# Kernel optimization log

Measured on AMD Instinct MI355X. Metric: run time of the kernel, lower is better.

The kernel has to match this reference:

```python
import jax, jax.numpy as jnp
import numpy as np

QMAX = 255.0  # bit=8 unsigned activation range


def ste_round(x):
    # straight-through round: exact integer rounding in fwd, identity grad
    return x + jax.lax.stop_gradient(jnp.round(x) - x)


def conv3x3(x, w, stride=1):
    return jax.lax.conv_general_dilated(
        x, w, window_strides=(stride, stride), padding=((1, 1), (1, 1)),
        dimension_numbers=('NCHW', 'OIHW', 'NCHW'))


def setup_inputs() -> dict:
    key = jax.random.key(0)
    k0, k1, k2 = jax.random.split(key, 3)
    N, C, H, W = 64, 256, 28, 28
    # uint8 activations and int8 (symmetric) weights, stored as integer-valued fp32
    x = jax.random.randint(k0, (N, C, H, W), 0, 256).astype(jnp.float32)
    w1 = jax.random.randint(k1, (C, C, 3, 3), -128, 128).astype(jnp.float32)
    w2 = jax.random.randint(k2, (C, C, 3, 3), -128, 128).astype(jnp.float32)
    f = jnp.float32
    return dict(
        x=x, w1=w1, w2=w2,
        s_x=f(0.05), z_x=f(128.0),
        s_w1=f(0.01), s_conv1=f(0.08), z_conv1=f(120.0),
        s_w2=f(0.01), s_conv2=f(0.07), z_conv2=f(130.0),
        s_add=f(0.09), z_add=f(125.0))


def qconv(x_q, w_q, s_in, z_in, s_w, s_out, z_out, stride=1):
    # integer-arithmetic conv: sum((x - z_in) * w) then requantize
    acc = conv3x3(x_q - z_in, w_q, stride)
    M = s_in * s_w / s_out  # per-cluster requant multiplier (cluster 0)
    return jnp.clip(ste_round(M * acc) + z_out, 0.0, QMAX)


def qadd(a, s_a, z_a, b, s_b, z_b, s_out, z_out):
    # fused dequant of both branches + residual add + requant
    y = (s_a / s_out) * (a - z_a) + (s_b / s_out) * (b - z_b)
    return jnp.clip(ste_round(y) + z_out, 0.0, QMAX)


def reference(x, w1, w2, s_x, z_x, s_w1, s_conv1, z_conv1,
              s_w2, s_conv2, z_conv2, s_add, z_add):
    out = qconv(x, w1, s_x, z_x, s_w1, s_conv1, z_conv1)          # conv1
    out = qconv(out, w2, s_conv1, z_conv1, s_w2, s_conv2, z_conv2)  # conv2
    return qadd(x, s_x, z_x, out, s_conv2, z_conv2, s_add, z_add)   # shortcut
```

## Files before the change

kernel.cpp:

```cpp
#include <hip/hip_runtime.h>
#include <stdint.h>

#define HWP 784
#define NPOS 50176
#define PLN ((size_t)NPOS * 64)
#define PAD_OFF 47616

typedef int   int4v   __attribute__((ext_vector_type(4)));
typedef int   int16v  __attribute__((ext_vector_type(16)));
typedef float float4v __attribute__((ext_vector_type(4)));
using as1_cv = const __attribute__((address_space(1))) void;
using as3_v  = __attribute__((address_space(3))) void;

__global__ __launch_bounds__(256) void k_nhwc(const float* __restrict__ x,
                                              int8_t* __restrict__ x8) {
    __shared__ int lA[256 * 15];
    __shared__ __align__(16) int lB[56 * 68];
    const int tid = threadIdx.x;
    const int P0 = blockIdx.x * 56;
    const int n = P0 / HWP;
    const int hw0 = P0 % HWP;
    const float* xb = x + (size_t)n * 256 * HWP + hw0;
#pragma unroll
    for (int k = 0; k < 14; ++k) {
        int e = tid + k * 256;
        int c = e / 14, pq = e % 14;
        float4v v = *(const float4v*)(xb + (size_t)c * HWP + pq * 4);
        int b0 = ((int)v[0] - 128) & 255;
        int b1 = ((int)v[1] - 128) & 255;
        int b2 = ((int)v[2] - 128) & 255;
        int b3 = ((int)v[3] - 128) & 255;
        lA[c * 15 + pq] = b0 | (b1 << 8) | (b2 << 16) | (b3 << 24);
    }
    __syncthreads();
#pragma unroll
    for (int k = 0; k < 4; ++k) {
        int u = tid + k * 256;
        if (u < 896) {
            int cg = u / 14, pq = u % 14;
            int d0 = lA[(cg * 4 + 0) * 15 + pq];
            int d1 = lA[(cg * 4 + 1) * 15 + pq];
            int d2 = lA[(cg * 4 + 2) * 15 + pq];
            int d3 = lA[(cg * 4 + 3) * 15 + pq];
#pragma unroll
            for (int j = 0; j < 4; ++j) {
                int sh = j * 8;
                int o = ((d0 >> sh) & 255) | (((d1 >> sh) & 255) << 8)
                      | (((d2 >> sh) & 255) << 16) | (((d3 >> sh) & 255) << 24);
                lB[(pq * 4 + j) * 68 + cg] = o;
            }
        }
    }
    __syncthreads();
#pragma unroll
    for (int k = 0; k < 4; ++k) {
        int ch = tid + k * 256;
        if (ch < 896) {
            int g = ch / 224, rem = ch % 224;
            int pos = rem >> 2, c4 = rem & 3;
            int4v val = *(const int4v*)&lB[pos * 68 + g * 16 + c4 * 4];
            *(int4v*)(x8 + (size_t)g * PLN + (size_t)(P0 + pos) * 64 + c4 * 16) = val;
        }
    }
}

__global__ __launch_bounds__(256) void k_w_prep(const float* __restrict__ w,
                                                int8_t* __restrict__ w8,
                                                int* __restrict__ wsum) {
    __shared__ int red[256];
    const int oc = blockIdx.x;
    const int t = threadIdx.x;
    const float* src = w + (size_t)oc * 2304 + (size_t)t * 9;
    const int g = oc >> 5;
    const int l = ((t >> 4) & 1) * 32 + (oc & 31);
    const int j = t & 15;
    const int s2 = (t >> 5) & 1;
    const int kb = t >> 6;
    int acc = 0;
#pragma unroll
    for (int tap = 0; tap < 9; ++tap) {
        int wv = (int)src[tap];
        acc += wv;
        int oo = ((((tap * 4 + kb) * 2 + s2) * 8 + g) * 64 + l) * 16 + j;
        w8[oo] = (int8_t)wv;
    }
    red[t] = acc;
    __syncthreads();
    for (int st = 128; st > 0; st >>= 1) {
        if (t < st) red[t] += red[t + st];
        __syncthreads();
    }
    if (t == 0) wsum[oc] = red[0];
}

template<bool FUSED>
__global__ __launch_bounds__(256, 3) void k_qconv_t(const int8_t* __restrict__ in8,
        const int8_t* __restrict__ w8, const int* __restrict__ wsum,
        const float* __restrict__ s_in_p, const float* __restrict__ s_w_p,
        const float* __restrict__ s_out_p, const float* __restrict__ z_in_p,
        const float* __restrict__ z_out_p, int8_t* __restrict__ out8,
        const int8_t* __restrict__ x8, const float* __restrict__ sxp,
        const float* __restrict__ zxp, const float* __restrict__ sap,
        const float* __restrict__ zap, float* __restrict__ outf) {
    __shared__ __align__(16) int8_t slab[47872];
    const int tid = threadIdx.x;
    const int lane = tid & 63;
    const int half = lane >> 5;
    const int wv = tid >> 6;
    const int wq = wv >> 1;
    const int wo = wv & 1;
    const int p0 = blockIdx.x * 128;
    const int gB = blockIdx.y * 128;

#pragma unroll
    for (int k = 0; k < 12; ++k) {
        int chunkid = tid + k * 256;
        if (chunkid < 2976) {
            int q = chunkid >> 4;
            int cs = chunkid & 15;
            int cg = cs ^ (q & 15);
            int qg = p0 - 29 + q;
            qg = qg < 0 ? 0 : (qg > NPOS - 1 ? NPOS - 1 : qg);
            const int8_t* src = in8 + (size_t)(cg >> 2) * PLN
                                    + (size_t)qg * 64 + (cg & 3) * 16;
            __builtin_amdgcn_global_load_lds((as1_cv*)src,
                                             (as3_v*)&slab[chunkid * 16], 16, 0, 0);
        }
    }

    const int zi = (int)z_in_p[0] - 128;
    const int spl = (zi & 0xff) * 0x01010101;
    if (tid < 16) {
        int4v pv; pv[0] = spl; pv[1] = spl; pv[2] = spl; pv[3] = spl;
        *(int4v*)&slab[PAD_OFF + tid * 16] = pv;
    }

    int rowpos[2], ph[2], pw[2];
#pragma unroll
    for (int mt = 0; mt < 2; ++mt) {
        rowpos[mt] = wq * 64 + mt * 32 + (lane & 31);
        int p = p0 + rowpos[mt];
        int hw = p % HWP;
        ph[mt] = hw / 28;
        pw[mt] = hw % 28;
    }
    int abz[9][2];
#pragma unroll
    for (int tap = 0; tap < 9; ++tap) {
        const int dh = tap / 3 - 1;
        const int dw = tap % 3 - 1;
#pragma unroll
        for (int mt = 0; mt < 2; ++mt) {
            int q = rowpos[mt] + dh * 28 + dw + 29;
            bool ok = ((unsigned)(ph[mt] + dh) < 28u) & ((unsigned)(pw[mt] + dw) < 28u);
            int base = ok ? (q << 8) : PAD_OFF;
            abz[tap][mt] = base ^ ((q & 15) << 4) ^ (half << 4);
        }
    }

    int16v acc[2][2];
#pragma unroll
    for (int mt = 0; mt < 2; ++mt)
#pragma unroll
        for (int nt = 0; nt < 2; ++nt)
#pragma unroll
            for (int r = 0; r < 16; ++r) acc[mt][nt][r] = 0;

    const int gg0 = blockIdx.y * 4 + wo * 2;
    const int8_t* wlane = w8 + gg0 * 1024 + lane * 16;

    int4v areg[2][2][2];
    int4v breg[2][2][2];

#define LOADB(u, slot)                                                      \
    {   const int8_t* wb_ = wlane + (size_t)(u) * 16384;                    \
        breg[slot][0][0] = *(const int4v*)(wb_);                            \
        breg[slot][1][0] = *(const int4v*)(wb_ + 1024);                     \
        breg[slot][0][1] = *(const int4v*)(wb_ + 8192);                     \
        breg[slot][1][1] = *(const int4v*)(wb_ + 9216); }
#define LOADA(u, slot)                                                      \
    {   const int tap_ = (u) >> 2, kb_ = (u) & 3;                           \
        areg[slot][0][0] = *(const int4v*)&slab[abz[tap_][0] ^ ((kb_*4+0)<<4)]; \
        areg[slot][0][1] = *(const int4v*)&slab[abz[tap_][0] ^ ((kb_*4+2)<<4)]; \
        areg[slot][1][0] = *(const int4v*)&slab[abz[tap_][1] ^ ((kb_*4+0)<<4)]; \
        areg[slot][1][1] = *(const int4v*)&slab[abz[tap_][1] ^ ((kb_*4+2)<<4)]; }

    LOADB(0, 0);

    __syncthreads();

    LOADA(0, 0);
#pragma unroll
    for (int u = 0; u < 36; ++u) {
        if (u < 35) {
            LOADA(u + 1, (u + 1) & 1);
            LOADB(u + 1, (u + 1) & 1);
        }
        const int sl = u & 1;
#pragma unroll
        for (int s = 0; s < 2; ++s)
#pragma unroll
            for (int mt = 0; mt < 2; ++mt)
#pragma unroll
                for (int nt = 0; nt < 2; ++nt)
                    acc[mt][nt] = __builtin_amdgcn_mfma_i32_32x32x32_i8(
                        areg[sl][mt][s], breg[sl][nt][s], acc[mt][nt], 0, 0, 0);
    }
#undef LOADA
#undef LOADB

    const float Mf = s_in_p[0] * s_w_p[0] / s_out_p[0];
    const float zof = z_out_p[0];
    const int zoffi = 128 - (int)z_in_p[0];
    const int plane = blockIdx.y * 2 + wo;

    if (!FUSED) {
        int8_t* o8p = out8 + (size_t)plane * PLN;
#pragma unroll
        for (int mt = 0; mt < 2; ++mt)
#pragma unroll
            for (int nt = 0; nt < 2; ++nt) {
                int oc = gB + wo * 64 + nt * 32 + (lane & 31);
                int corr = zoffi * wsum[oc];
#pragma unroll
                for (int r = 0; r < 16; ++r) {
                    int prow = (r & 3) + 8 * (r >> 2) + 4 * half;
                    int pos = p0 + wq * 64 + mt * 32 + prow;
                    float q = rintf(Mf * (float)(acc[mt][nt][r] + corr)) + zof;
                    q = fminf(fmaxf(q, 0.0f), 255.0f);
                    o8p[(size_t)pos * 64 + nt * 32 + (lane & 31)] = (int8_t)((int)q - 128);
                }
            }
    } else {
        const float ra = sxp[0] / sap[0];
        const float rb = s_out_p[0] / sap[0];
        const float zx = zxp[0];
        const float z2 = z_out_p[0];
        const float za = zap[0];
        __syncthreads();
        float* tp = (float*)slab + wv * 2080;
        const int pl = lane & 31;
#pragma unroll
        for (int mt = 0; mt < 2; ++mt) {
#pragma unroll
            for (int nt = 0; nt < 2; ++nt) {
                int oc = gB + wo * 64 + nt * 32 + (lane & 31);
                int corr = zoffi * wsum[oc];
#pragma unroll
                for (int r = 0; r < 16; ++r) {
                    int prow = (r & 3) + 8 * (r >> 2) + 4 * half;
                    float q2 = rintf(Mf * (float)(acc[mt][nt][r] + corr)) + zof;
                    q2 = fminf(fmaxf(q2, 0.0f), 255.0f);
                    tp[prow * 65 + nt * 32 + (lane & 31)] = q2;
                }
            }
            const int pglob = p0 + wq * 64 + mt * 32 + pl;
            const int n = pglob / HWP;
            const int hwo = pglob % HWP;
            const int8_t* x8p = x8 + (size_t)plane * PLN + (size_t)pglob * 64 + half * 32;
            int4v r0 = *(const int4v*)x8p;
            int4v r1 = *(const int4v*)(x8p + 16);
            int xb[8];
            xb[0] = r0[0]; xb[1] = r0[1]; xb[2] = r0[2]; xb[3] = r0[3];
            xb[4] = r1[0]; xb[5] = r1[1]; xb[6] = r1[2]; xb[7] = r1[3];
            float* obase = outf + ((size_t)(n * 256 + gB + wo * 64 + half * 32)) * HWP + hwo;
#pragma unroll
            for (int j = 0; j < 32; ++j) {
                int bv = (xb[j >> 2] >> ((j & 3) * 8)) & 255;
                int xval = (int)(int8_t)bv + 128;
                float q2 = tp[pl * 65 + half * 32 + j];
                float y = ra * ((float)xval - zx) + rb * (q2 - z2);
                float qf = rintf(y) + za;
                qf = fminf(fmaxf(qf, 0.0f), 255.0f);
                obase[(size_t)j * HWP] = qf;
            }
        }
    }
}

extern "C" void kernel_launch(void* const* d_in, const int* in_sizes, int n_in,
                              void* d_out, int out_size, void* d_ws, size_t ws_size,
                              hipStream_t stream) {
    (void)in_sizes; (void)n_in; (void)out_size; (void)ws_size;
    const float* x    = (const float*)d_in[0];
    const float* w1   = (const float*)d_in[1];
    const float* w2   = (const float*)d_in[2];
    const float* s_x  = (const float*)d_in[3];
    const float* z_x  = (const float*)d_in[4];
    const float* s_w1 = (const float*)d_in[5];
    const float* s_c1 = (const float*)d_in[6];
    const float* z_c1 = (const float*)d_in[7];
    const float* s_w2 = (const float*)d_in[8];
    const float* s_c2 = (const float*)d_in[9];
    const float* z_c2 = (const float*)d_in[10];
    const float* s_ad = (const float*)d_in[11];
    const float* z_ad = (const float*)d_in[12];
    float* out = (float*)d_out;

    int8_t* ws    = (int8_t*)d_ws;
    int8_t* x8    = ws;
    int8_t* o1    = ws + 12845056;
    int8_t* w8a   = ws + 25690112;
    int8_t* w8b   = ws + 26279936;
    int*    wsum1 = (int*)(ws + 26869760);
    int*    wsum2 = (int*)(ws + 26870784);

    k_nhwc<<<896, 256, 0, stream>>>(x, x8);
    k_w_prep<<<256, 256, 0, stream>>>(w1, w8a, wsum1);
    k_w_prep<<<256, 256, 0, stream>>>(w2, w8b, wsum2);
    k_qconv_t<false><<<dim3(392, 2), 256, 0, stream>>>(x8, w8a, wsum1,
        s_x, s_w1, s_c1, z_x, z_c1, o1,
        nullptr, nullptr, nullptr, nullptr, nullptr, nullptr);
    k_qconv_t<true><<<dim3(392, 2), 256, 0, stream>>>(o1, w8b, wsum2,
        s_c1, s_w2, s_c2, z_c1, z_c2, nullptr,
        x8, s_x, z_x, s_ad, z_ad, out);
}
```

Measured before the change: 217.1 us.

## Deepen weight prefetch, stage conv1 output through LDS, merge weight prep launches

The weight-fragment register pipeline in the int8 MFMA conv loop goes from double to triple buffering, so B loads are issued two iterations ahead and global latency is better hidden. The conv1 epilogue now writes requantized bytes into an LDS tile and stores 16-byte vectors per position instead of scattered byte stores. The two weight-prep launches are merged into one grid. The extra register buffers raise VGPR pressure and may reduce occupancy, and the LDS staging adds a barrier.

```diff
diff --git a/kernel.cpp b/kernel.cpp
--- a/kernel.cpp
+++ b/kernel.cpp
@@ -64,11 +64,18 @@
     }
 }
 
-__global__ __launch_bounds__(256) void k_w_prep(const float* __restrict__ w,
-                                                int8_t* __restrict__ w8,
-                                                int* __restrict__ wsum) {
+__global__ __launch_bounds__(256) void k_w_prep(const float* __restrict__ wa,
+                                                const float* __restrict__ wb,
+                                                int8_t* __restrict__ w8a,
+                                                int8_t* __restrict__ w8b,
+                                                int* __restrict__ wsa,
+                                                int* __restrict__ wsb) {
     __shared__ int red[256];
-    const int oc = blockIdx.x;
+    const int which = blockIdx.x >> 8;
+    const int oc = blockIdx.x & 255;
+    const float* w = which ? wb : wa;
+    int8_t* w8 = which ? w8b : w8a;
+    int* wsum = which ? wsb : wsa;
     const int t = threadIdx.x;
     const float* src = w + (size_t)oc * 2304 + (size_t)t * 9;
     const int g = oc >> 5;
@@ -170,7 +177,7 @@
     const int8_t* wlane = w8 + gg0 * 1024 + lane * 16;
 
     int4v areg[2][2][2];
-    int4v breg[2][2][2];
+    int4v breg[3][2][2];
 
 #define LOADB(u, slot)                                                      \
     {   const int8_t* wb_ = wlane + (size_t)(u) * 16384;                    \
@@ -186,17 +193,17 @@
         areg[slot][1][1] = *(const int4v*)&slab[abz[tap_][1] ^ ((kb_*4+2)<<4)]; }
 
     LOADB(0, 0);
+    LOADB(1, 1);
 
     __syncthreads();
 
     LOADA(0, 0);
 #pragma unroll
     for (int u = 0; u < 36; ++u) {
-        if (u < 35) {
-            LOADA(u + 1, (u + 1) & 1);
-            LOADB(u + 1, (u + 1) & 1);
-        }
+        if (u < 34) LOADB(u + 2, (u + 2) % 3);
+        if (u < 35) LOADA(u + 1, (u + 1) & 1);
         const int sl = u & 1;
+        const int bs = u % 3;
 #pragma unroll
         for (int s = 0; s < 2; ++s)
 #pragma unroll
@@ -204,7 +211,7 @@
 #pragma unroll
                 for (int nt = 0; nt < 2; ++nt)
                     acc[mt][nt] = __builtin_amdgcn_mfma_i32_32x32x32_i8(
-                        areg[sl][mt][s], breg[sl][nt][s], acc[mt][nt], 0, 0, 0);
+                        areg[sl][mt][s], breg[bs][nt][s], acc[mt][nt], 0, 0, 0);
     }
 #undef LOADA
 #undef LOADB
@@ -215,7 +222,8 @@
     const int plane = blockIdx.y * 2 + wo;
 
     if (!FUSED) {
-        int8_t* o8p = out8 + (size_t)plane * PLN;
+        __syncthreads();
+        int8_t* tpb = slab + wv * 5120;
 #pragma unroll
         for (int mt = 0; mt < 2; ++mt)
 #pragma unroll
@@ -225,12 +233,17 @@
 #pragma unroll
                 for (int r = 0; r < 16; ++r) {
                     int prow = (r & 3) + 8 * (r >> 2) + 4 * half;
-                    int pos = p0 + wq * 64 + mt * 32 + prow;
+                    int pl = mt * 32 + prow;
                     float q = rintf(Mf * (float)(acc[mt][nt][r] + corr)) + zof;
                     q = fminf(fmaxf(q, 0.0f), 255.0f);
-                    o8p[(size_t)pos * 64 + nt * 32 + (lane & 31)] = (int8_t)((int)q - 128);
+                    tpb[pl * 80 + nt * 32 + (lane & 31)] = (int8_t)((int)q - 128);
                 }
             }
+        int8_t* o8p = out8 + (size_t)plane * PLN + (size_t)(p0 + wq * 64 + lane) * 64;
+        const int8_t* rowp = tpb + lane * 80;
+#pragma unroll
+        for (int k = 0; k < 4; ++k)
+            *(int4v*)(o8p + k * 16) = *(const int4v*)(rowp + k * 16);
     } else {
         const float ra = sxp[0] / sap[0];
         const float rb = s_out_p[0] / sap[0];
@@ -306,8 +319,7 @@
     int*    wsum2 = (int*)(ws + 26870784);
 
     k_nhwc<<<896, 256, 0, stream>>>(x, x8);
-    k_w_prep<<<256, 256, 0, stream>>>(w1, w8a, wsum1);
-    k_w_prep<<<256, 256, 0, stream>>>(w2, w8b, wsum2);
+    k_w_prep<<<512, 256, 0, stream>>>(w1, w2, w8a, w8b, wsum1, wsum2);
     k_qconv_t<false><<<dim3(392, 2), 256, 0, stream>>>(x8, w8a, wsum1,
         s_x, s_w1, s_c1, z_x, z_c1, o1,
         nullptr, nullptr, nullptr, nullptr, nullptr, nullptr);
```

Result: no change. 212.8 us (-2.0%).
